# Kernel optimization log

Hardware: AMD Instinct MI355X
Metric: run time of the kernel (lower is better)

The kernel has to match this reference:

```python
import jax, jax.numpy as jnp
import numpy as np

EPS0 = 1.0          # epsilon_0 > 0 branch: h = h + eps0 * h_w
N_ITERS = 5         # number_of_iterations
EPS = 1e-20


def setup_inputs() -> dict:
    key = jax.random.key(0)
    k1, k2 = jax.random.split(key)
    # nonnegative input (NMF assumes nonnegative data)
    x = jax.random.uniform(k1, (4, 64, 32, 32), dtype=jnp.float32)
    # weights uniform in [0,1), then column-normalized as the weights.setter does
    w = jax.random.uniform(k2, (64, 96), dtype=jnp.float32)
    w = w / w.sum(axis=0, keepdims=True)
    # h_initial uniform 1/number_of_neurons (set_h_init_to_uniform)
    h0 = jnp.full((96,), 1.0 / 96.0, dtype=jnp.float32)
    return {"x": x, "weights": w, "h_initial": h0}


def reference(x, weights, h_initial):
    # x: (B, Cin, H, W); weights: (Cin, Cout); h_initial: (Cout,)
    B, Cin, H, W = x.shape
    Cout = weights.shape[1]
    # h = tile(h_initial) -> (B, Cout, H, W)
    h = jnp.broadcast_to(h_initial[None, :, None, None], (B, Cout, H, W))
    for _ in range(N_ITERS):
        # (B, Cin, Cout, H, W) broadcast product
        hw = h[:, None, :, :, :] * weights[None, :, :, None, None]
        hw = hw / (hw.sum(axis=2, keepdims=True) + EPS)   # normalize over Cout
        hw = (hw * x[:, :, None, :, :]).sum(axis=1)        # reduce Cin -> (B, Cout, H, W)
        h = h + EPS0 * hw                                  # epsilon_0 > 0 path
        h = h / (h.sum(axis=1, keepdims=True) + EPS)       # normalize over Cout
    return h
```

## Files before the change

kernel.cpp:

```cpp
#include <hip/hip_runtime.h>

#define CIN 64
#define COUT 96
#define HW_  1024
#define NTHR 512
#define NITER 5
#define NMF_EPS 1e-20f

typedef short bf16x8 __attribute__((ext_vector_type(8)));
typedef float f32x4  __attribute__((ext_vector_type(4)));

__device__ __forceinline__ unsigned short bf_hi(float x) {
    return (unsigned short)(__float_as_uint(x) >> 16);
}
__device__ __forceinline__ float bf_f(unsigned short u) {
    return __uint_as_float(((unsigned int)u) << 16);
}
__device__ __forceinline__ unsigned short bf_rn(float x) {
    unsigned int b = __float_as_uint(x);
    b += 0x7FFF + ((b >> 16) & 1);
    return (unsigned short)(b >> 16);
}
__device__ __forceinline__ void split8(const float* v, bf16x8& hi, bf16x8& lo) {
    #pragma unroll
    for (int e = 0; e < 8; ++e) {
        const unsigned short h = bf_hi(v[e]);
        hi[e] = (short)h;
        lo[e] = (short)bf_rn(v[e] - bf_f(h));
    }
}

__global__ __launch_bounds__(NTHR) void nmf_kernel(
    const float* __restrict__ x,
    const float* __restrict__ w,
    const float* __restrict__ h0,
    float* __restrict__ out)
{
    __shared__ unsigned short Hb_hi[16][104], Hb_lo[16][104];
    __shared__ unsigned short Tb_hi[16][72],  Tb_lo[16][72];
    __shared__ float Par[6][16];

    const int t    = threadIdx.x;
    const int wid  = t >> 6;
    const int l    = t & 63;
    const int px   = l & 15;
    const int quad = l >> 4;
    const int tile = blockIdx.x;
    const int b    = tile >> 6;
    const int hw0  = (tile & 63) << 4;

    for (int k = t; k < 16 * COUT; k += NTHR) {
        const int p = k / COUT;
        const int j = k - p * COUT;
        const float v = h0[j];
        const unsigned short hi = bf_hi(v);
        Hb_hi[p][j] = hi;
        Hb_lo[p][j] = bf_rn(v - bf_f(hi));
    }

    bf16x8 a1h0, a1l0, a1h1, a1l1, a1h2, a1l2;
    if (wid < 4) {
        const float* wrow = &w[(wid * 16 + px) * COUT + quad * 8];
        float v[8];
        #pragma unroll
        for (int e = 0; e < 8; ++e) v[e] = wrow[e];
        split8(v, a1h0, a1l0);
        #pragma unroll
        for (int e = 0; e < 8; ++e) v[e] = wrow[32 + e];
        split8(v, a1h1, a1l1);
        #pragma unroll
        for (int e = 0; e < 8; ++e) v[e] = wrow[64 + e];
        split8(v, a1h2, a1l2);
    }
    bf16x8 a2h0, a2l0, a2h1, a2l1;
    const int j0s2 = wid * 16 + quad * 4;
    if (wid < 6) {
        const int jcol = wid * 16 + px;
        float v[8];
        #pragma unroll
        for (int e = 0; e < 8; ++e) v[e] = w[(quad * 8 + e) * COUT + jcol];
        split8(v, a2h0, a2l0);
        #pragma unroll
        for (int e = 0; e < 8; ++e) v[e] = w[(32 + quad * 8 + e) * COUT + jcol];
        split8(v, a2h1, a2l1);
    }

    float xq0 = 0.f, xq1 = 0.f, xq2 = 0.f, xq3 = 0.f;
    if (wid < 4) {
        const size_t base = ((size_t)b * CIN + wid * 16 + quad * 4) * HW_ + hw0 + px;
        xq0 = x[base]; xq1 = x[base + HW_]; xq2 = x[base + 2 * HW_]; xq3 = x[base + 3 * HW_];
    }
    float hr0 = 0.f, hr1 = 0.f, hr2 = 0.f, hr3 = 0.f;
    if (wid < 6) {
        hr0 = h0[j0s2]; hr1 = h0[j0s2 + 1]; hr2 = h0[j0s2 + 2]; hr3 = h0[j0s2 + 3];
    }
    __syncthreads();

    #pragma unroll 1
    for (int it = 0; it < NITER; ++it) {
        if (wid < 4) {
            f32x4 acc = {0.f, 0.f, 0.f, 0.f};
            {
                const bf16x8 bh = *(const bf16x8*)&Hb_hi[px][quad * 8];
                const bf16x8 bl = *(const bf16x8*)&Hb_lo[px][quad * 8];
                acc = __builtin_amdgcn_mfma_f32_16x16x32_bf16(a1h0, bh, acc, 0, 0, 0);
                acc = __builtin_amdgcn_mfma_f32_16x16x32_bf16(a1l0, bh, acc, 0, 0, 0);
                acc = __builtin_amdgcn_mfma_f32_16x16x32_bf16(a1h0, bl, acc, 0, 0, 0);
            }
            {
                const bf16x8 bh = *(const bf16x8*)&Hb_hi[px][32 + quad * 8];
                const bf16x8 bl = *(const bf16x8*)&Hb_lo[px][32 + quad * 8];
                acc = __builtin_amdgcn_mfma_f32_16x16x32_bf16(a1h1, bh, acc, 0, 0, 0);
                acc = __builtin_amdgcn_mfma_f32_16x16x32_bf16(a1l1, bh, acc, 0, 0, 0);
                acc = __builtin_amdgcn_mfma_f32_16x16x32_bf16(a1h1, bl, acc, 0, 0, 0);
            }
            {
                const bf16x8 bh = *(const bf16x8*)&Hb_hi[px][64 + quad * 8];
                const bf16x8 bl = *(const bf16x8*)&Hb_lo[px][64 + quad * 8];
                acc = __builtin_amdgcn_mfma_f32_16x16x32_bf16(a1h2, bh, acc, 0, 0, 0);
                acc = __builtin_amdgcn_mfma_f32_16x16x32_bf16(a1l2, bh, acc, 0, 0, 0);
                acc = __builtin_amdgcn_mfma_f32_16x16x32_bf16(a1h2, bl, acc, 0, 0, 0);
            }
            const float t0 = xq0 * __builtin_amdgcn_rcpf(acc[0] + NMF_EPS);
            const float t1 = xq1 * __builtin_amdgcn_rcpf(acc[1] + NMF_EPS);
            const float t2 = xq2 * __builtin_amdgcn_rcpf(acc[2] + NMF_EPS);
            const float t3 = xq3 * __builtin_amdgcn_rcpf(acc[3] + NMF_EPS);
            const int i0 = wid * 16 + quad * 4;
            ushort4 th, tl;
            th.x = bf_hi(t0); tl.x = bf_rn(t0 - bf_f(th.x));
            th.y = bf_hi(t1); tl.y = bf_rn(t1 - bf_f(th.y));
            th.z = bf_hi(t2); tl.z = bf_rn(t2 - bf_f(th.z));
            th.w = bf_hi(t3); tl.w = bf_rn(t3 - bf_f(th.w));
            *(ushort4*)&Tb_hi[px][i0] = th;
            *(ushort4*)&Tb_lo[px][i0] = tl;
        }
        __syncthreads();

        float hp0 = 0.f, hp1 = 0.f, hp2 = 0.f, hp3 = 0.f;
        if (wid < 6) {
            f32x4 acc = {0.f, 0.f, 0.f, 0.f};
            {
                const bf16x8 bh = *(const bf16x8*)&Tb_hi[px][quad * 8];
                const bf16x8 bl = *(const bf16x8*)&Tb_lo[px][quad * 8];
                acc = __builtin_amdgcn_mfma_f32_16x16x32_bf16(a2h0, bh, acc, 0, 0, 0);
                acc = __builtin_amdgcn_mfma_f32_16x16x32_bf16(a2l0, bh, acc, 0, 0, 0);
                acc = __builtin_amdgcn_mfma_f32_16x16x32_bf16(a2h0, bl, acc, 0, 0, 0);
            }
            {
                const bf16x8 bh = *(const bf16x8*)&Tb_hi[px][32 + quad * 8];
                const bf16x8 bl = *(const bf16x8*)&Tb_lo[px][32 + quad * 8];
                acc = __builtin_amdgcn_mfma_f32_16x16x32_bf16(a2h1, bh, acc, 0, 0, 0);
                acc = __builtin_amdgcn_mfma_f32_16x16x32_bf16(a2l1, bh, acc, 0, 0, 0);
                acc = __builtin_amdgcn_mfma_f32_16x16x32_bf16(a2h1, bl, acc, 0, 0, 0);
            }
            hp0 = hr0 * (1.f + acc[0]);
            hp1 = hr1 * (1.f + acc[1]);
            hp2 = hr2 * (1.f + acc[2]);
            hp3 = hr3 * (1.f + acc[3]);
            float s = (hp0 + hp1) + (hp2 + hp3);
            s += __shfl_xor(s, 16, 64);
            s += __shfl_xor(s, 32, 64);
            if (l < 16) Par[wid][l] = s;
        }
        __syncthreads();

        if (wid < 6) {
            const float tot = NMF_EPS +
                ((Par[0][px] + Par[1][px]) + (Par[2][px] + Par[3][px])) +
                (Par[4][px] + Par[5][px]);
            const float inv = __builtin_amdgcn_rcpf(tot);
            hr0 = hp0 * inv; hr1 = hp1 * inv; hr2 = hp2 * inv; hr3 = hp3 * inv;
            if (it < NITER - 1) {
                ushort4 hh, hl;
                hh.x = bf_hi(hr0); hl.x = bf_rn(hr0 - bf_f(hh.x));
                hh.y = bf_hi(hr1); hl.y = bf_rn(hr1 - bf_f(hh.y));
                hh.z = bf_hi(hr2); hl.z = bf_rn(hr2 - bf_f(hh.z));
                hh.w = bf_hi(hr3); hl.w = bf_rn(hr3 - bf_f(hh.w));
                *(ushort4*)&Hb_hi[px][j0s2] = hh;
                *(ushort4*)&Hb_lo[px][j0s2] = hl;
            }
        }
        __syncthreads();
    }

    if (wid < 6) {
        const size_t base = ((size_t)b * COUT + j0s2) * HW_ + hw0 + px;
        out[base]           = hr0;
        out[base + HW_]     = hr1;
        out[base + 2 * HW_] = hr2;
        out[base + 3 * HW_] = hr3;
    }
}

extern "C" void kernel_launch(void* const* d_in, const int* in_sizes, int n_in,
                              void* d_out, int out_size, void* d_ws, size_t ws_size,
                              hipStream_t stream) {
    const float* x  = (const float*)d_in[0];
    const float* w  = (const float*)d_in[1];
    const float* h0 = (const float*)d_in[2];
    float* out = (float*)d_out;
    nmf_kernel<<<256, NTHR, 0, stream>>>(x, w, h0, out);
}
```

Measured before the change: 12.38 us.

## Defer per-pixel normalization via scale invariance and split MFMA accumulators

The per-iteration normalization of h is dropped and h is kept unnormalized. The first stage is scale-invariant in h, so folding the previous column sum S into x keeps the update exact, and the final output is normalized once at the end. This removes one __syncthreads barrier and the Par reduction phase from every iteration. The MFMA chains are also split across independent accumulators to shorten dependency latency. The cost is that unnormalized h can grow across iterations, which may change bf16 hi/lo split precision.

```diff
diff --git a/kernel.cpp b/kernel.cpp
--- a/kernel.cpp
+++ b/kernel.cpp
@@ -90,41 +90,51 @@
         const size_t base = ((size_t)b * CIN + wid * 16 + quad * 4) * HW_ + hw0 + px;
         xq0 = x[base]; xq1 = x[base + HW_]; xq2 = x[base + 2 * HW_]; xq3 = x[base + 3 * HW_];
     }
-    float hr0 = 0.f, hr1 = 0.f, hr2 = 0.f, hr3 = 0.f;
+    float gr0 = 0.f, gr1 = 0.f, gr2 = 0.f, gr3 = 0.f;
     if (wid < 6) {
-        hr0 = h0[j0s2]; hr1 = h0[j0s2 + 1]; hr2 = h0[j0s2 + 2]; hr3 = h0[j0s2 + 3];
+        gr0 = h0[j0s2]; gr1 = h0[j0s2 + 1]; gr2 = h0[j0s2 + 2]; gr3 = h0[j0s2 + 3];
+        float s = (gr0 + gr1) + (gr2 + gr3);
+        s += __shfl_xor(s, 16, 64);
+        s += __shfl_xor(s, 32, 64);
+        if (l < 16) Par[wid][l] = s;
     }
     __syncthreads();
 
     #pragma unroll 1
     for (int it = 0; it < NITER; ++it) {
         if (wid < 4) {
-            f32x4 acc = {0.f, 0.f, 0.f, 0.f};
+            const float S = ((Par[0][px] + Par[1][px]) + (Par[2][px] + Par[3][px]))
+                          + (Par[4][px] + Par[5][px]);
+            f32x4 acc0 = {0.f, 0.f, 0.f, 0.f}, acc1 = acc0, acc2 = acc0;
             {
                 const bf16x8 bh = *(const bf16x8*)&Hb_hi[px][quad * 8];
                 const bf16x8 bl = *(const bf16x8*)&Hb_lo[px][quad * 8];
-                acc = __builtin_amdgcn_mfma_f32_16x16x32_bf16(a1h0, bh, acc, 0, 0, 0);
-                acc = __builtin_amdgcn_mfma_f32_16x16x32_bf16(a1l0, bh, acc, 0, 0, 0);
-                acc = __builtin_amdgcn_mfma_f32_16x16x32_bf16(a1h0, bl, acc, 0, 0, 0);
+                acc0 = __builtin_amdgcn_mfma_f32_16x16x32_bf16(a1h0, bh, acc0, 0, 0, 0);
+                acc1 = __builtin_amdgcn_mfma_f32_16x16x32_bf16(a1l0, bh, acc1, 0, 0, 0);
+                acc2 = __builtin_amdgcn_mfma_f32_16x16x32_bf16(a1h0, bl, acc2, 0, 0, 0);
             }
             {
                 const bf16x8 bh = *(const bf16x8*)&Hb_hi[px][32 + quad * 8];
                 const bf16x8 bl = *(const bf16x8*)&Hb_lo[px][32 + quad * 8];
-                acc = __builtin_amdgcn_mfma_f32_16x16x32_bf16(a1h1, bh, acc, 0, 0, 0);
-                acc = __builtin_amdgcn_mfma_f32_16x16x32_bf16(a1l1, bh, acc, 0, 0, 0);
-                acc = __builtin_amdgcn_mfma_f32_16x16x32_bf16(a1h1, bl, acc, 0, 0, 0);
+                acc0 = __builtin_amdgcn_mfma_f32_16x16x32_bf16(a1h1, bh, acc0, 0, 0, 0);
+                acc1 = __builtin_amdgcn_mfma_f32_16x16x32_bf16(a1l1, bh, acc1, 0, 0, 0);
+                acc2 = __builtin_amdgcn_mfma_f32_16x16x32_bf16(a1h1, bl, acc2, 0, 0, 0);
             }
             {
                 const bf16x8 bh = *(const bf16x8*)&Hb_hi[px][64 + quad * 8];
                 const bf16x8 bl = *(const bf16x8*)&Hb_lo[px][64 + quad * 8];
-                acc = __builtin_amdgcn_mfma_f32_16x16x32_bf16(a1h2, bh, acc, 0, 0, 0);
-                acc = __builtin_amdgcn_mfma_f32_16x16x32_bf16(a1l2, bh, acc, 0, 0, 0);
-                acc = __builtin_amdgcn_mfma_f32_16x16x32_bf16(a1h2, bl, acc, 0, 0, 0);
-            }
-            const float t0 = xq0 * __builtin_amdgcn_rcpf(acc[0] + NMF_EPS);
-            const float t1 = xq1 * __builtin_amdgcn_rcpf(acc[1] + NMF_EPS);
-            const float t2 = xq2 * __builtin_amdgcn_rcpf(acc[2] + NMF_EPS);
-            const float t3 = xq3 * __builtin_amdgcn_rcpf(acc[3] + NMF_EPS);
+                acc0 = __builtin_amdgcn_mfma_f32_16x16x32_bf16(a1h2, bh, acc0, 0, 0, 0);
+                acc1 = __builtin_amdgcn_mfma_f32_16x16x32_bf16(a1l2, bh, acc1, 0, 0, 0);
+                acc2 = __builtin_amdgcn_mfma_f32_16x16x32_bf16(a1h2, bl, acc2, 0, 0, 0);
+            }
+            const float d0 = (acc0[0] + acc1[0]) + acc2[0];
+            const float d1 = (acc0[1] + acc1[1]) + acc2[1];
+            const float d2 = (acc0[2] + acc1[2]) + acc2[2];
+            const float d3 = (acc0[3] + acc1[3]) + acc2[3];
+            const float t0 = (xq0 * S) * __builtin_amdgcn_rcpf(d0 + NMF_EPS);
+            const float t1 = (xq1 * S) * __builtin_amdgcn_rcpf(d1 + NMF_EPS);
+            const float t2 = (xq2 * S) * __builtin_amdgcn_rcpf(d2 + NMF_EPS);
+            const float t3 = (xq3 * S) * __builtin_amdgcn_rcpf(d3 + NMF_EPS);
             const int i0 = wid * 16 + quad * 4;
             ushort4 th, tl;
             th.x = bf_hi(t0); tl.x = bf_rn(t0 - bf_f(th.x));
@@ -136,59 +146,52 @@
         }
         __syncthreads();
 
-        float hp0 = 0.f, hp1 = 0.f, hp2 = 0.f, hp3 = 0.f;
         if (wid < 6) {
-            f32x4 acc = {0.f, 0.f, 0.f, 0.f};
+            f32x4 acc0 = {0.f, 0.f, 0.f, 0.f}, acc1 = acc0;
             {
                 const bf16x8 bh = *(const bf16x8*)&Tb_hi[px][quad * 8];
                 const bf16x8 bl = *(const bf16x8*)&Tb_lo[px][quad * 8];
-                acc = __builtin_amdgcn_mfma_f32_16x16x32_bf16(a2h0, bh, acc, 0, 0, 0);
-                acc = __builtin_amdgcn_mfma_f32_16x16x32_bf16(a2l0, bh, acc, 0, 0, 0);
-                acc = __builtin_amdgcn_mfma_f32_16x16x32_bf16(a2h0, bl, acc, 0, 0, 0);
+                acc0 = __builtin_amdgcn_mfma_f32_16x16x32_bf16(a2h0, bh, acc0, 0, 0, 0);
+                acc1 = __builtin_amdgcn_mfma_f32_16x16x32_bf16(a2l0, bh, acc1, 0, 0, 0);
+                acc0 = __builtin_amdgcn_mfma_f32_16x16x32_bf16(a2h0, bl, acc0, 0, 0, 0);
             }
             {
                 const bf16x8 bh = *(const bf16x8*)&Tb_hi[px][32 + quad * 8];
                 const bf16x8 bl = *(const bf16x8*)&Tb_lo[px][32 + quad * 8];
-                acc = __builtin_amdgcn_mfma_f32_16x16x32_bf16(a2h1, bh, acc, 0, 0, 0);
-                acc = __builtin_amdgcn_mfma_f32_16x16x32_bf16(a2l1, bh, acc, 0, 0, 0);
-                acc = __builtin_amdgcn_mfma_f32_16x16x32_bf16(a2h1, bl, acc, 0, 0, 0);
-            }
-            hp0 = hr0 * (1.f + acc[0]);
-            hp1 = hr1 * (1.f + acc[1]);
-            hp2 = hr2 * (1.f + acc[2]);
-            hp3 = hr3 * (1.f + acc[3]);
-            float s = (hp0 + hp1) + (hp2 + hp3);
+                acc0 = __builtin_amdgcn_mfma_f32_16x16x32_bf16(a2h1, bh, acc0, 0, 0, 0);
+                acc1 = __builtin_amdgcn_mfma_f32_16x16x32_bf16(a2l1, bh, acc1, 0, 0, 0);
+                acc0 = __builtin_amdgcn_mfma_f32_16x16x32_bf16(a2h1, bl, acc0, 0, 0, 0);
+            }
+            gr0 = gr0 * (1.f + (acc0[0] + acc1[0]));
+            gr1 = gr1 * (1.f + (acc0[1] + acc1[1]));
+            gr2 = gr2 * (1.f + (acc0[2] + acc1[2]));
+            gr3 = gr3 * (1.f + (acc0[3] + acc1[3]));
+            float s = (gr0 + gr1) + (gr2 + gr3);
             s += __shfl_xor(s, 16, 64);
             s += __shfl_xor(s, 32, 64);
             if (l < 16) Par[wid][l] = s;
+            if (it < NITER - 1) {
+                ushort4 hh, hl;
+                hh.x = bf_hi(gr0); hl.x = bf_rn(gr0 - bf_f(hh.x));
+                hh.y = bf_hi(gr1); hl.y = bf_rn(gr1 - bf_f(hh.y));
+                hh.z = bf_hi(gr2); hl.z = bf_rn(gr2 - bf_f(hh.z));
+                hh.w = bf_hi(gr3); hl.w = bf_rn(gr3 - bf_f(hh.w));
+                *(ushort4*)&Hb_hi[px][j0s2] = hh;
+                *(ushort4*)&Hb_lo[px][j0s2] = hl;
+            }
         }
         __syncthreads();
-
-        if (wid < 6) {
-            const float tot = NMF_EPS +
-                ((Par[0][px] + Par[1][px]) + (Par[2][px] + Par[3][px])) +
-                (Par[4][px] + Par[5][px]);
-            const float inv = __builtin_amdgcn_rcpf(tot);
-            hr0 = hp0 * inv; hr1 = hp1 * inv; hr2 = hp2 * inv; hr3 = hp3 * inv;
-            if (it < NITER - 1) {
-                ushort4 hh, hl;
-                hh.x = bf_hi(hr0); hl.x = bf_rn(hr0 - bf_f(hh.x));
-                hh.y = bf_hi(hr1); hl.y = bf_rn(hr1 - bf_f(hh.y));
-                hh.z = bf_hi(hr2); hl.z = bf_rn(hr2 - bf_f(hh.z));
-                hh.w = bf_hi(hr3); hl.w = bf_rn(hr3 - bf_f(hh.w));
-                *(ushort4*)&Hb_hi[px][j0s2] = hh;
-                *(ushort4*)&Hb_lo[px][j0s2] = hl;
-            }
-        }
-        __syncthreads();
     }
 
     if (wid < 6) {
+        const float Sf = ((Par[0][px] + Par[1][px]) + (Par[2][px] + Par[3][px]))
+                       + (Par[4][px] + Par[5][px]) + NMF_EPS;
+        const float inv = __builtin_amdgcn_rcpf(Sf);
         const size_t base = ((size_t)b * COUT + j0s2) * HW_ + hw0 + px;
-        out[base]           = hr0;
-        out[base + HW_]     = hr1;
-        out[base + 2 * HW_] = hr2;
-        out[base + 3 * HW_] = hr3;
+        out[base]           = gr0 * inv;
+        out[base + HW_]     = gr1 * inv;
+        out[base + 2 * HW_] = gr2 * inv;
+        out[base + 3 * HW_] = gr3 * inv;
     }
 }
 
```

Result: faster. 11.65 us (-5.9%).
